# Performance work log

Hardware: AMD Instinct MI355X
Metric: run time of the kernel (lower is better)

## Reference

```python
import jax, jax.numpy as jnp
import numpy as np

K = 20
NEG_SLOPE = 0.2


def knn_idx(x, k):
    # squared euclidean pairwise distances [N, N]
    sq = jnp.sum(x * x, axis=-1)
    d = sq[:, None] - 2.0 * (x @ x.T) + sq[None, :]
    _, idx = jax.lax.top_k(-d, k)  # k nearest (self included, dist 0)
    return idx  # [N, k]


def edge_conv(x, W, b, k):
    # Dynamic EdgeConv: kNN on current features, gather, concat[x_i, x_j - x_i], MLP, max over neighbors
    idx = knn_idx(x, k)                 # [N, k]
    xj = x[idx]                         # [N, k, C] gather
    xi = jnp.broadcast_to(x[:, None, :], xj.shape)
    e = jnp.concatenate([xi, xj - xi], axis=-1)   # [N, k, 2C]
    h = jax.nn.leaky_relu(jnp.einsum('nkc,cf->nkf', e, W) + b, NEG_SLOPE)
    return jnp.max(h, axis=1)           # [N, F] max-aggregation


def setup_inputs() -> dict:
    key = jax.random.key(0)
    ks = jax.random.split(key, 7)
    N, C_in, H, F_out = 16384, 3, 64, 128
    def lin(k1, k2, fan_in, fan_out):
        lim = 1.0 / np.sqrt(fan_in)
        W = jax.random.uniform(k1, (fan_in, fan_out), jnp.float32, -lim, lim)
        b = jax.random.uniform(k2, (fan_out,), jnp.float32, -lim, lim)
        return W, b
    x = jax.random.normal(ks[0], (N, C_in), jnp.float32)
    W1, b1 = lin(ks[1], ks[2], 2 * C_in, H)
    W2, b2 = lin(ks[3], ks[4], 2 * H, H)
    W3, b3 = lin(ks[5], ks[6], 2 * H, F_out)
    return {"x": x, "W1": W1, "b1": b1, "W2": W2, "b2": b2, "W3": W3, "b3": b3}


def reference(x, W1, b1, W2, b2, W3, b3):
    h = edge_conv(x, W1, b1, K)
    h = edge_conv(h, W2, b2, K)
    h = edge_conv(h, W3, b3, K)
    return h
```

## Files before the change

### kernel.cpp

```cpp
#include <hip/hip_runtime.h>
#include <math.h>

#define K_NN 20
#define NEG_SLOPE 0.2f

constexpr int NSEG1 = 8;
constexpr int NSEG  = 8;
constexpr int BKT   = 16;
constexpr int OCAP  = 2048;

__device__ __forceinline__ void insert_sorted(float (&dl)[K_NN], int (&il)[K_NN],
                                              float d, int idx) {
    if (d < dl[K_NN - 1]) {
        dl[K_NN - 1] = d; il[K_NN - 1] = idx;
#pragma unroll
        for (int p = K_NN - 1; p > 0; --p) {
            if (dl[p] < dl[p - 1]) {
                float td = dl[p]; dl[p] = dl[p - 1]; dl[p - 1] = td;
                int   ti = il[p]; il[p] = il[p - 1]; il[p - 1] = ti;
            }
        }
    }
}

template<int C>
__global__ __launch_bounds__(256) void sqnorm_kernel(const float* __restrict__ x,
                                                     float* __restrict__ sq, int N) {
    int i = blockIdx.x * 256 + threadIdx.x;
    if (i < N) {
        float s = 0.f;
#pragma unroll
        for (int c = 0; c < C; ++c) { float v = x[i * C + c]; s += v * v; }
        sq[i] = s;
    }
}

__global__ __launch_bounds__(256) void pack3_kernel(const float* __restrict__ x,
                                                    float4* __restrict__ x4, int N) {
    int i = blockIdx.x * 256 + threadIdx.x;
    if (i < N) {
        float a = x[i * 3], b = x[i * 3 + 1], c = x[i * 3 + 2];
        float s = a * a; s += b * b; s += c * c;
        x4[i] = make_float4(a, b, c, s);
    }
}

__global__ __launch_bounds__(128) void tau3_kernel(const float4* __restrict__ x4,
                                                   float* __restrict__ tau, int N) {
    __shared__ float bufD[16 * 128];
    __shared__ int   bufI[16 * 128];
    const int tid = threadIdx.x;
    const int q   = blockIdx.x * 128 + tid;
    const float4 qv = x4[q];

    float dl[K_NN]; int il[K_NN];
#pragma unroll
    for (int p = 0; p < K_NN; ++p) { dl[p] = __builtin_inff(); il[p] = 0; }
    int cnt = 0;

    for (int j0 = 0; j0 < 2048; j0 += 8) {
#pragma unroll
        for (int u = 0; u < 8; ++u) {
            float4 pv = x4[j0 + u];
            float dot = qv.x * pv.x; dot += qv.y * pv.y; dot += qv.z * pv.z;
            float d = (qv.w - 2.f * dot) + pv.w;
            if (d < dl[K_NN - 1]) { bufD[tid + 128 * cnt] = d; bufI[tid + 128 * cnt] = j0 + u; ++cnt; }
        }
        if (__any(cnt >= 8)) {
            for (int u2 = 0; u2 < cnt; ++u2)
                insert_sorted(dl, il, bufD[tid + 128 * u2], bufI[tid + 128 * u2]);
            cnt = 0;
        }
    }
    for (int u2 = 0; u2 < cnt; ++u2)
        insert_sorted(dl, il, bufD[tid + 128 * u2], bufI[tid + 128 * u2]);

    tau[q] = dl[K_NN - 1] * 1.000002f + 2e-6f * qv.w;
}

__global__ __launch_bounds__(64) void knn3z_kernel(const float4* __restrict__ x4,
                                                   const float* __restrict__ tau,
                                                   float* __restrict__ pdist,
                                                   int* __restrict__ pidx, int N) {
    __shared__ float4 tile4[128];
    __shared__ float bufD[16 * 64];
    __shared__ int   bufI[16 * 64];
    const int t   = threadIdx.x;
    const int q   = blockIdx.x * 64 + t;
    const int seg = blockIdx.y;
    const int segLen = N / NSEG1;
    const int j0  = seg * segLen;

    const float4 qv = x4[q];
    const float  tq = tau[q];

    float dl[K_NN]; int il[K_NN];
#pragma unroll
    for (int p = 0; p < K_NN; ++p) { dl[p] = __builtin_inff(); il[p] = 0; }
    int cnt = 0;

    for (int t0 = 0; t0 < segLen; t0 += 128) {
        tile4[t]      = x4[j0 + t0 + t];
        tile4[t + 64] = x4[j0 + t0 + t + 64];
        for (int jj = 0; jj < 128; jj += 8) {
#pragma unroll
            for (int u = 0; u < 8; ++u) {
                float4 pv = tile4[jj + u];
                float dot = qv.x * pv.x; dot += qv.y * pv.y; dot += qv.z * pv.z;
                float d = (qv.w - 2.f * dot) + pv.w;
                if (d <= tq && d < dl[K_NN - 1]) {
                    bufD[t + 64 * cnt] = d;
                    bufI[t + 64 * cnt] = j0 + t0 + jj + u;
                    ++cnt;
                }
            }
            if (__any(cnt >= 8)) {
                for (int u2 = 0; u2 < cnt; ++u2)
                    insert_sorted(dl, il, bufD[t + 64 * u2], bufI[t + 64 * u2]);
                cnt = 0;
            }
        }
    }
    for (int u2 = 0; u2 < cnt; ++u2)
        insert_sorted(dl, il, bufD[t + 64 * u2], bufI[t + 64 * u2]);

    const size_t base = ((size_t)q * NSEG1 + seg) * K_NN;
#pragma unroll
    for (int p = 0; p < K_NN; ++p) { pdist[base + p] = dl[p]; pidx[base + p] = il[p]; }
}

__global__ __launch_bounds__(256) void tau64_kernel(const float* __restrict__ feat,
                                                    const float* __restrict__ sq,
                                                    const int* __restrict__ knn,
                                                    float* __restrict__ tau, int N) {
    int q = blockIdx.x * 256 + threadIdx.x;
    if (q >= N) return;
    const float4* qrow = (const float4*)&feat[(size_t)q * 64];
    float4 qf[16];
#pragma unroll
    for (int m = 0; m < 16; ++m) qf[m] = qrow[m];
    const float qsq = sq[q];
    float t = 0.f;
    for (int k = 0; k < K_NN; ++k) {
        int j = knn[(size_t)q * K_NN + k];
        const float4* prow = (const float4*)&feat[(size_t)j * 64];
        float dot = 0.f;
#pragma unroll
        for (int m = 0; m < 16; ++m) {
            float4 pv = prow[m];
            dot += qf[m].x * pv.x; dot += qf[m].y * pv.y;
            dot += qf[m].z * pv.z; dot += qf[m].w * pv.w;
        }
        float d = (qsq - 2.f * dot) + sq[j];
        t = fmaxf(t, d);
    }
    tau[q] = t * 1.000002f + 2e-6f * qsq;
}

__global__ __launch_bounds__(256) void transpose64_kernel(const float* __restrict__ xin,
                                                          float* __restrict__ xT, int N) {
    int i = blockIdx.x * 256 + threadIdx.x;
    int c = blockIdx.y;
    xT[(size_t)c * N + i] = xin[(size_t)i * 64 + c];
}

__global__ __launch_bounds__(256, 2) void fused64v_kernel(const float* __restrict__ xT,
                                                          const float* __restrict__ sq,
                                                          const float* __restrict__ tau,
                                                          float* __restrict__ pdist,
                                                          int* __restrict__ pidx,
                                                          uint2* __restrict__ ovG, int N) {
    __shared__ float qT[64][36];
    __shared__ float pT[2][8][256];
    __shared__ float bktD[BKT][32];
    __shared__ int   bktI[BKT][32];
    __shared__ float lstD[K_NN][32];
    __shared__ int   lstI[K_NN][32];
    __shared__ int   qn[32];
    __shared__ float thr_s[32];
    __shared__ int   ovf;
    __shared__ int   ovn;

    const int tid  = threadIdx.x;
    const int lane = tid & 63;
    const int w    = tid >> 6;
    const int q0   = blockIdx.x * 32;
    const int seg  = blockIdx.y;
    const int segLen = N / NSEG;
    const int j0   = seg * segLen;
    uint2* ovB = ovG + (size_t)(seg * gridDim.x + blockIdx.x) * OCAP;

    const int rw = w * 2;
    const int cl = lane * 4;

    {
        int c = tid >> 2, qq = (tid & 3) * 8;
        *(float4*)&qT[c][qq]     = *(const float4*)&xT[(size_t)c * N + q0 + qq];
        *(float4*)&qT[c][qq + 4] = *(const float4*)&xT[(size_t)c * N + q0 + qq + 4];
    }
    if (tid < 32) {
        qn[tid] = 0; thr_s[tid] = __builtin_inff();
#pragma unroll
        for (int p = 0; p < K_NN; ++p) { lstD[p][tid] = __builtin_inff(); lstI[p][tid] = 0x7fffffff; }
    }
    if (tid == 0) { ovf = 0; ovn = 0; }

    float qsv[8], qtau[8], thr_c[8];
    *(float4*)&qsv[0]  = *(const float4*)&sq[q0 + w * 8];
    *(float4*)&qsv[4]  = *(const float4*)&sq[q0 + w * 8 + 4];
    *(float4*)&qtau[0] = *(const float4*)&tau[q0 + w * 8];
    *(float4*)&qtau[4] = *(const float4*)&tau[q0 + w * 8 + 4];
#pragma unroll
    for (int i = 0; i < 8; ++i) thr_c[i] = __builtin_inff();

    {
        float4 a = *(const float4*)&xT[(size_t)(rw)     * N + j0 + cl];
        float4 b = *(const float4*)&xT[(size_t)(rw + 1) * N + j0 + cl];
        *(float4*)&pT[0][rw][cl]     = a;
        *(float4*)&pT[0][rw + 1][cl] = b;
    }
    __syncthreads();

    const int nT = segLen / 256;
    int buf = 0;
    for (int t = 0; t < nT; ++t) {
        const int jb = j0 + t * 256;
        float acc[8][4];
#pragma unroll
        for (int i = 0; i < 8; ++i)
#pragma unroll
            for (int j = 0; j < 4; ++j) acc[i][j] = 0.f;

        for (int cc = 0; cc < 8; ++cc) {
            const bool last = (t == nT - 1) && (cc == 7);
            float4 na, nb;
            if (!last) {
                const int ncc = (cc + 1) & 7;
                const int njb = (cc == 7) ? jb + 256 : jb;
                na = *(const float4*)&xT[(size_t)(ncc * 8 + rw)     * N + njb + cl];
                nb = *(const float4*)&xT[(size_t)(ncc * 8 + rw + 1) * N + njb + cl];
            }
#pragma unroll
            for (int c8 = 0; c8 < 8; ++c8) {
                const int c = cc * 8 + c8;
                float4 qa = *(const float4*)&qT[c][w * 8];
                float4 qb = *(const float4*)&qT[c][w * 8 + 4];
                float4 pv = *(const float4*)&pT[buf][c8][cl];
                float qf[8] = {qa.x, qa.y, qa.z, qa.w, qb.x, qb.y, qb.z, qb.w};
                float pf[4] = {pv.x, pv.y, pv.z, pv.w};
#pragma unroll
                for (int i = 0; i < 8; ++i)
#pragma unroll
                    for (int j = 0; j < 4; ++j) acc[i][j] += qf[i] * pf[j];
            }
            if (!last) {
                *(float4*)&pT[buf ^ 1][rw][cl]     = na;
                *(float4*)&pT[buf ^ 1][rw + 1][cl] = nb;
            }
            __syncthreads();
            buf ^= 1;
        }

        float psv[4];
        *(float4*)&psv[0] = *(const float4*)&sq[jb + cl];
        const int tbase = t * 256;
#pragma unroll
        for (int i = 0; i < 8; ++i) {
#pragma unroll
            for (int j = 0; j < 4; ++j) {
                float d = (qsv[i] - 2.f * acc[i][j]) + psv[j];
                if (d <= qtau[i] && d < thr_c[i]) {
                    int slot = atomicAdd(&qn[w * 8 + i], 1);
                    if (slot < BKT) {
                        bktD[slot][w * 8 + i] = d;
                        bktI[slot][w * 8 + i] = tbase + cl + j;
                    } else {
                        int os = atomicAdd(&ovn, 1);
                        if (os < OCAP)
                            ovB[os] = make_uint2(__float_as_uint(d),
                                (unsigned)(((w * 8 + i) << 11) | (tbase + cl + j)));
                        ovf = 1;
                    }
                }
            }
        }
        __syncthreads();
        const int doDrain = ovf;
        __syncthreads();
        if (doDrain) {
            if (tid < 32) {
                int c = qn[tid]; c = (c < BKT) ? c : BKT;
                for (int s = 0; s < c; ++s) {
                    float d = bktD[s][tid]; int idx = j0 + bktI[s][tid];
                    float td = lstD[K_NN - 1][tid]; int ti = lstI[K_NN - 1][tid];
                    if (d < td || (d == td && idx < ti)) {
                        lstD[K_NN - 1][tid] = d; lstI[K_NN - 1][tid] = idx;
#pragma unroll
                        for (int p = K_NN - 1; p > 0; --p) {
                            float a = lstD[p][tid], b = lstD[p - 1][tid];
                            int  ai = lstI[p][tid], bi = lstI[p - 1][tid];
                            if (a < b || (a == b && ai < bi)) {
                                lstD[p][tid] = b; lstD[p - 1][tid] = a;
                                lstI[p][tid] = bi; lstI[p - 1][tid] = ai;
                            } else break;
                        }
                    }
                }
                qn[tid] = 0;
                thr_s[tid] = lstD[K_NN - 1][tid];
            }
            if (tid == 0) ovf = 0;
            __syncthreads();
        }
#pragma unroll
        for (int i = 0; i < 8; ++i) thr_c[i] = thr_s[w * 8 + i];
    }

    if (tid < 32) {
        int c = qn[tid]; c = (c < BKT) ? c : BKT;
        int tot = ovn; tot = (tot < OCAP) ? tot : OCAP;
        for (int s = 0; s < c + tot; ++s) {
            float d; int idx;
            if (s < c) { d = bktD[s][tid]; idx = j0 + bktI[s][tid]; }
            else {
                uint2 v = ovB[s - c];
                if ((int)(v.y >> 11) != tid) continue;
                d = __uint_as_float(v.x); idx = j0 + (int)(v.y & 2047u);
            }
            float td = lstD[K_NN - 1][tid]; int ti = lstI[K_NN - 1][tid];
            if (d < td || (d == td && idx < ti)) {
                lstD[K_NN - 1][tid] = d; lstI[K_NN - 1][tid] = idx;
#pragma unroll
                for (int p = K_NN - 1; p > 0; --p) {
                    float a = lstD[p][tid], b = lstD[p - 1][tid];
                    int  ai = lstI[p][tid], bi = lstI[p - 1][tid];
                    if (a < b || (a == b && ai < bi)) {
                        lstD[p][tid] = b; lstD[p - 1][tid] = a;
                        lstI[p][tid] = bi; lstI[p - 1][tid] = ai;
                    } else break;
                }
            }
        }
        const size_t base = ((size_t)(q0 + tid) * NSEG + seg) * K_NN;
#pragma unroll
        for (int p = 0; p < K_NN; ++p) { pdist[base + p] = lstD[p][tid]; pidx[base + p] = lstI[p][tid]; }
    }
}

__global__ __launch_bounds__(256) void knn_merge_kernel(const float* __restrict__ pdist,
                                                        const int* __restrict__ pidx,
                                                        int* __restrict__ knn,
                                                        int N, int nseg) {
    int q = blockIdx.x * 256 + threadIdx.x;
    if (q >= N) return;
    float dl[K_NN]; int il[K_NN];
#pragma unroll
    for (int p = 0; p < K_NN; ++p) { dl[p] = __builtin_inff(); il[p] = 0; }

    for (int s = 0; s < nseg; ++s) {
        const long base = ((long)q * nseg + s) * K_NN;
        for (int p = 0; p < K_NN; ++p) {
            float d = pdist[base + p];
            if (!(d < dl[K_NN - 1])) break;
            insert_sorted(dl, il, d, pidx[base + p]);
        }
    }
#pragma unroll
    for (int p = 0; p < K_NN; ++p) knn[(long)q * K_NN + p] = il[p];
}

template<int C, int F>
__global__ __launch_bounds__(256) void proj_kernel(const float* __restrict__ x,
                                                   const float* __restrict__ W,
                                                   const float* __restrict__ b,
                                                   float* __restrict__ A,
                                                   float* __restrict__ U, int N) {
    int gid = blockIdx.x * 256 + threadIdx.x;
    int i = gid / F, f = gid % F;
    if (i >= N) return;
    float a = b[f], u = 0.f;
#pragma unroll
    for (int c = 0; c < C; ++c) {
        float xv = x[i * C + c];
        a += xv * W[c * F + f];
        u += xv * W[(C + c) * F + f];
    }
    A[(long)i * F + f] = a;
    U[(long)i * F + f] = u;
}

template<int F>
__global__ __launch_bounds__(256) void agg_kernel(const float* __restrict__ A,
                                                  const float* __restrict__ U,
                                                  const int* __restrict__ knn,
                                                  float* __restrict__ out, int N) {
    int gid = blockIdx.x * 256 + threadIdx.x;
    int i = gid / F, f = gid % F;
    if (i >= N) return;
    float a = A[(long)i * F + f] - U[(long)i * F + f];
    float m = -__builtin_inff();
#pragma unroll
    for (int k = 0; k < K_NN; ++k) {
        int j = knn[(long)i * K_NN + k];
        float v = a + U[(long)j * F + f];
        v = fmaxf(v, v * NEG_SLOPE);
        m = fmaxf(m, v);
    }
    out[(long)i * F + f] = m;
}

extern "C" void kernel_launch(void* const* d_in, const int* in_sizes, int n_in,
                              void* d_out, int out_size, void* d_ws, size_t ws_size,
                              hipStream_t stream) {
    const float* x  = (const float*)d_in[0];
    const float* W1 = (const float*)d_in[1];
    const float* b1 = (const float*)d_in[2];
    const float* W2 = (const float*)d_in[3];
    const float* b2 = (const float*)d_in[4];
    const float* W3 = (const float*)d_in[5];
    const float* b3 = (const float*)d_in[6];
    const int N = in_sizes[0] / 3;

    float* ws  = (float*)d_ws;
    float* sq  = ws;
    float* A   = sq + N;
    float* U   = A + (size_t)N * 128;
    float* h1  = U + (size_t)N * 128;
    float* h2  = h1 + (size_t)N * 64;
    float4* x4 = (float4*)(h2 + (size_t)N * 64);
    float* xT  = (float*)(x4 + N);
    float* tau = xT + (size_t)N * 64;
    float* pd  = tau + N;
    int* pidx  = (int*)(pd + (size_t)N * NSEG1 * K_NN);
    int* knn   = pidx + (size_t)N * NSEG1 * K_NN;
    uint2* ovG = (uint2*)(knn + (size_t)N * K_NN);
    float* out = (float*)d_out;

    const int qBlocks = N / 256;

    pack3_kernel<<<qBlocks, 256, 0, stream>>>(x, x4, N);
    tau3_kernel<<<N / 128, 128, 0, stream>>>(x4, tau, N);
    knn3z_kernel<<<dim3(N / 64, NSEG1), 64, 0, stream>>>(x4, tau, pd, pidx, N);
    knn_merge_kernel<<<qBlocks, 256, 0, stream>>>(pd, pidx, knn, N, NSEG1);
    proj_kernel<3, 64><<<(N * 64) / 256, 256, 0, stream>>>(x, W1, b1, A, U, N);
    agg_kernel<64><<<(N * 64) / 256, 256, 0, stream>>>(A, U, knn, h1, N);

    sqnorm_kernel<64><<<qBlocks, 256, 0, stream>>>(h1, sq, N);
    transpose64_kernel<<<dim3(qBlocks, 64), 256, 0, stream>>>(h1, xT, N);
    tau64_kernel<<<qBlocks, 256, 0, stream>>>(h1, sq, knn, tau, N);
    fused64v_kernel<<<dim3(N / 32, NSEG), 256, 0, stream>>>(xT, sq, tau, pd, pidx, ovG, N);
    knn_merge_kernel<<<qBlocks, 256, 0, stream>>>(pd, pidx, knn, N, NSEG);
    proj_kernel<64, 64><<<(N * 64) / 256, 256, 0, stream>>>(h1, W2, b2, A, U, N);
    agg_kernel<64><<<(N * 64) / 256, 256, 0, stream>>>(A, U, knn, h2, N);

    sqnorm_kernel<64><<<qBlocks, 256, 0, stream>>>(h2, sq, N);
    transpose64_kernel<<<dim3(qBlocks, 64), 256, 0, stream>>>(h2, xT, N);
    tau64_kernel<<<qBlocks, 256, 0, stream>>>(h2, sq, knn, tau, N);
    fused64v_kernel<<<dim3(N / 32, NSEG), 256, 0, stream>>>(xT, sq, tau, pd, pidx, ovG, N);
    knn_merge_kernel<<<qBlocks, 256, 0, stream>>>(pd, pidx, knn, N, NSEG);
    proj_kernel<64, 128><<<(N * 128) / 256, 256, 0, stream>>>(h2, W3, b3, A, U, N);
    agg_kernel<128><<<(N * 128) / 256, 256, 0, stream>>>(A, U, knn, out, N);
}
```

Measured before the change: 2.062 ms.

## Stage 64-dim kNN point tiles via direct global-to-LDS loads in 32-channel halves

Result: no change. 2.031 ms (-1.5%).

```diff
diff --git a/kernel.cpp b/kernel.cpp
--- a/kernel.cpp
+++ b/kernel.cpp
@@ -6,8 +6,14 @@
 
 constexpr int NSEG1 = 8;
 constexpr int NSEG  = 8;
-constexpr int BKT   = 16;
+constexpr int BKT   = 8;
 constexpr int OCAP  = 2048;
+
+__device__ __forceinline__ void gload16(const float* g, float* l) {
+    __builtin_amdgcn_global_load_lds(
+        (const __attribute__((address_space(1))) void*)g,
+        (__attribute__((address_space(3))) void*)l, 16, 0, 0);
+}
 
 __device__ __forceinline__ void insert_sorted(float (&dl)[K_NN], int (&il)[K_NN],
                                               float d, int idx) {
@@ -164,14 +170,14 @@
     xT[(size_t)c * N + i] = xin[(size_t)i * 64 + c];
 }
 
-__global__ __launch_bounds__(256, 2) void fused64v_kernel(const float* __restrict__ xT,
+__global__ __launch_bounds__(256, 2) void fused64g_kernel(const float* __restrict__ xT,
                                                           const float* __restrict__ sq,
                                                           const float* __restrict__ tau,
                                                           float* __restrict__ pdist,
                                                           int* __restrict__ pidx,
                                                           uint2* __restrict__ ovG, int N) {
-    __shared__ float qT[64][36];
-    __shared__ float pT[2][8][256];
+    __shared__ float pT[2][32][256];
+    __shared__ float qT[64][32];
     __shared__ float bktD[BKT][32];
     __shared__ int   bktI[BKT][32];
     __shared__ float lstD[K_NN][32];
@@ -190,7 +196,6 @@
     const int j0   = seg * segLen;
     uint2* ovB = ovG + (size_t)(seg * gridDim.x + blockIdx.x) * OCAP;
 
-    const int rw = w * 2;
     const int cl = lane * 4;
 
     {
@@ -213,17 +218,12 @@
 #pragma unroll
     for (int i = 0; i < 8; ++i) thr_c[i] = __builtin_inff();
 
-    {
-        float4 a = *(const float4*)&xT[(size_t)(rw)     * N + j0 + cl];
-        float4 b = *(const float4*)&xT[(size_t)(rw + 1) * N + j0 + cl];
-        *(float4*)&pT[0][rw][cl]     = a;
-        *(float4*)&pT[0][rw + 1][cl] = b;
-    }
+#pragma unroll
+    for (int k = 0; k < 8; ++k)
+        gload16(&xT[(size_t)(w * 8 + k) * N + j0 + cl], &pT[0][w * 8 + k][0]);
     __syncthreads();
 
-    const int nT = segLen / 256;
-    int buf = 0;
-    for (int t = 0; t < nT; ++t) {
+    for (int t = 0; t < 8; ++t) {
         const int jb = j0 + t * 256;
         float acc[8][4];
 #pragma unroll
@@ -231,18 +231,22 @@
 #pragma unroll
             for (int j = 0; j < 4; ++j) acc[i][j] = 0.f;
 
-        for (int cc = 0; cc < 8; ++cc) {
-            const bool last = (t == nT - 1) && (cc == 7);
-            float4 na, nb;
-            if (!last) {
-                const int ncc = (cc + 1) & 7;
-                const int njb = (cc == 7) ? jb + 256 : jb;
-                na = *(const float4*)&xT[(size_t)(ncc * 8 + rw)     * N + njb + cl];
-                nb = *(const float4*)&xT[(size_t)(ncc * 8 + rw + 1) * N + njb + cl];
-            }
-#pragma unroll
-            for (int c8 = 0; c8 < 8; ++c8) {
-                const int c = cc * 8 + c8;
+#pragma unroll
+        for (int h = 0; h < 2; ++h) {
+            const int g = 2 * t + h;
+            const int buf = g & 1;
+            if (g + 1 < 16) {
+                const int g2  = g + 1;
+                const int h2  = g2 & 1;
+                const int jb2 = j0 + (g2 >> 1) * 256;
+#pragma unroll
+                for (int k = 0; k < 8; ++k)
+                    gload16(&xT[(size_t)(h2 * 32 + w * 8 + k) * N + jb2 + cl],
+                            &pT[buf ^ 1][w * 8 + k][0]);
+            }
+#pragma unroll 8
+            for (int c8 = 0; c8 < 32; ++c8) {
+                const int c = h * 32 + c8;
                 float4 qa = *(const float4*)&qT[c][w * 8];
                 float4 qb = *(const float4*)&qT[c][w * 8 + 4];
                 float4 pv = *(const float4*)&pT[buf][c8][cl];
@@ -253,12 +257,7 @@
 #pragma unroll
                     for (int j = 0; j < 4; ++j) acc[i][j] += qf[i] * pf[j];
             }
-            if (!last) {
-                *(float4*)&pT[buf ^ 1][rw][cl]     = na;
-                *(float4*)&pT[buf ^ 1][rw + 1][cl] = nb;
-            }
-            __syncthreads();
-            buf ^= 1;
+            if (h == 0) __syncthreads();
         }
 
         float psv[4];
@@ -448,7 +447,7 @@
     sqnorm_kernel<64><<<qBlocks, 256, 0, stream>>>(h1, sq, N);
     transpose64_kernel<<<dim3(qBlocks, 64), 256, 0, stream>>>(h1, xT, N);
     tau64_kernel<<<qBlocks, 256, 0, stream>>>(h1, sq, knn, tau, N);
-    fused64v_kernel<<<dim3(N / 32, NSEG), 256, 0, stream>>>(xT, sq, tau, pd, pidx, ovG, N);
+    fused64g_kernel<<<dim3(N / 32, NSEG), 256, 0, stream>>>(xT, sq, tau, pd, pidx, ovG, N);
     knn_merge_kernel<<<qBlocks, 256, 0, stream>>>(pd, pidx, knn, N, NSEG);
     proj_kernel<64, 64><<<(N * 64) / 256, 256, 0, stream>>>(h1, W2, b2, A, U, N);
     agg_kernel<64><<<(N * 64) / 256, 256, 0, stream>>>(A, U, knn, h2, N);
@@ -456,7 +455,7 @@
     sqnorm_kernel<64><<<qBlocks, 256, 0, stream>>>(h2, sq, N);
     transpose64_kernel<<<dim3(qBlocks, 64), 256, 0, stream>>>(h2, xT, N);
     tau64_kernel<<<qBlocks, 256, 0, stream>>>(h2, sq, knn, tau, N);
-    fused64v_kernel<<<dim3(N / 32, NSEG), 256, 0, stream>>>(xT, sq, tau, pd, pidx, ovG, N);
+    fused64g_kernel<<<dim3(N / 32, NSEG), 256, 0, stream>>>(xT, sq, tau, pd, pidx, ovG, N);
     knn_merge_kernel<<<qBlocks, 256, 0, stream>>>(pd, pidx, knn, N, NSEG);
     proj_kernel<64, 128><<<(N * 128) / 256, 256, 0, stream>>>(h2, W3, b3, A, U, N);
     agg_kernel<128><<<(N * 128) / 256, 256, 0, stream>>>(A, U, knn, out, N);
```
